# Kernel tuning notes

Measured on AMD Instinct MI355X. Metric: run time of the kernel, lower is better.

The kernel has to match this reference:

```python
import jax, jax.numpy as jnp
import numpy as np

N_NODES = 100000
N_EDGES = 1600000
IN_FEAT = 50
HIDDEN = 64
N_CLASSES = 41


def setup_inputs() -> dict:
    key = jax.random.key(0)
    ks = jax.random.split(key, 8)
    x = jax.random.normal(ks[0], (N_NODES, IN_FEAT), dtype=jnp.float32)
    W1_l = jax.random.normal(ks[1], (IN_FEAT, HIDDEN), dtype=jnp.float32) * (1.0 / np.sqrt(IN_FEAT))
    W1_r = jax.random.normal(ks[2], (IN_FEAT, HIDDEN), dtype=jnp.float32) * (1.0 / np.sqrt(IN_FEAT))
    b1 = jnp.zeros((HIDDEN,), dtype=jnp.float32)
    W2_l = jax.random.normal(ks[3], (HIDDEN, N_CLASSES), dtype=jnp.float32) * (1.0 / np.sqrt(HIDDEN))
    W2_r = jax.random.normal(ks[4], (HIDDEN, N_CLASSES), dtype=jnp.float32) * (1.0 / np.sqrt(HIDDEN))
    b2 = jnp.zeros((N_CLASSES,), dtype=jnp.float32)
    src = jax.random.randint(ks[5], (N_EDGES,), 0, N_NODES, dtype=jnp.int64 if jax.config.jax_enable_x64 else jnp.int32)
    dst = jax.random.randint(ks[6], (N_EDGES,), 0, N_NODES, dtype=jnp.int64 if jax.config.jax_enable_x64 else jnp.int32)
    return {"x": x, "W1_l": W1_l, "W1_r": W1_r, "b1": b1,
            "W2_l": W2_l, "W2_r": W2_r, "b2": b2, "src": src, "dst": dst}


def _sage_conv(h, src, dst, W_l, W_r, b):
    # sum-aggregate neighbor features (message from src -> dst), then dense transform
    agg = jax.ops.segment_sum(h[src], dst, num_segments=N_NODES)  # [N, F]
    return agg @ W_l + h @ W_r + b


def reference(x, W1_l, W1_r, b1, W2_l, W2_r, b2, src, dst):
    h = _sage_conv(x, src, dst, W1_l, W1_r, b1)
    h = jax.nn.relu(h)
    # dropout is identity in eval mode
    o = _sage_conv(h, src, dst, W2_l, W2_r, b2)
    return jax.nn.log_softmax(o, axis=1)
```

## Files before the change

kernel.cpp:

```cpp
#include <hip/hip_runtime.h>
#include <hip/hip_bf16.h>
#include <math.h>

#define N_NODES   100000
#define N_EDGES   1600000
#define IN_FEAT   50
#define HIDDEN    64
#define N_CLASSES 41
#define NC48      48
#define N_TILES   (N_NODES / 16)

#define NPB   200
#define NBUK  (N_NODES / NPB)
#define BEPT  16
#define BA_BLOCKS ((N_EDGES + 256 * BEPT - 1) / (256 * BEPT))
#define SCAP  4096

#define PACKX_BLOCKS (N_NODES * 64 / 256)
#define PW_BLOCKS    28

typedef __attribute__((ext_vector_type(8))) _Float16 half8;
typedef __attribute__((ext_vector_type(4))) float   float4v;

union f16pk { _Float16 h[2]; unsigned u; };

__device__ __forceinline__ int clampidx(int i) {
  return ((unsigned)i < (unsigned)N_NODES) ? i : 0;
}

__device__ __forceinline__ void acc8(float* acc, half8 u, float one) {
#pragma unroll
  for (int t = 0; t < 8; ++t) acc[t] = fmaf((float)u[t], one, acc[t]);
}

__global__ __launch_bounds__(256) void prep_kernel(
    const float* __restrict__ x, _Float16* __restrict__ xh,
    const float* __restrict__ W1l, const float* __restrict__ W1r,
    const float* __restrict__ W2l, const float* __restrict__ W2r,
    unsigned* __restrict__ wt1l, unsigned* __restrict__ wt1r,
    unsigned* __restrict__ wt2l, unsigned* __restrict__ wt2r,
    int* __restrict__ bcnt, int* __restrict__ wcurrel,
    int* __restrict__ start) {
  if (blockIdx.x < PACKX_BLOCKS) {
    int i = blockIdx.x * 256 + threadIdx.x;
    int node = i >> 6, c = i & 63;
    xh[i] = (c < IN_FEAT) ? (_Float16)x[node * IN_FEAT + c] : (_Float16)0.f;
    return;
  }
  int tid = threadIdx.x;
  if (blockIdx.x == PACKX_BLOCKS) {
    bcnt[tid] = 0; bcnt[256 + tid] = 0;
    wcurrel[tid] = 0; wcurrel[256 + tid] = 0;
    if (tid == 0) start[N_NODES] = N_EDGES;
  }
  int i = (blockIdx.x - PACKX_BLOCKS) * 256 + tid;
  f16pk pk;
  if (i < 2048 * 2) {
    int which = i >> 11, j = i & 2047;
    int n = j >> 5, kp = j & 31;
    const float* W = which ? W1r : W1l;
    int k0 = 2 * kp, k1 = 2 * kp + 1;
    pk.h[0] = (_Float16)((k0 < IN_FEAT) ? W[k0 * HIDDEN + n] : 0.f);
    pk.h[1] = (_Float16)((k1 < IN_FEAT) ? W[k1 * HIDDEN + n] : 0.f);
    (which ? wt1r : wt1l)[j] = pk.u;
  } else if (i < 4096 + 2 * 1536) {
    int j = i - 4096;
    int which = (j >= 1536), jj = which ? j - 1536 : j;
    int n = jj >> 5, kp = jj & 31;
    const float* W = which ? W2r : W2l;
    pk.h[0] = (_Float16)((n < N_CLASSES) ? W[(2 * kp) * N_CLASSES + n] : 0.f);
    pk.h[1] = (_Float16)((n < N_CLASSES) ? W[(2 * kp + 1) * N_CLASSES + n] : 0.f);
    (which ? wt2r : wt2l)[jj] = pk.u;
  }
}

__global__ __launch_bounds__(256) void bhist_kernel(
    const int* __restrict__ dst, int* __restrict__ bcnt) {
  __shared__ int lh[NBUK];
  int tid = threadIdx.x;
  for (int i = tid; i < NBUK; i += 256) lh[i] = 0;
  __syncthreads();
  int base = blockIdx.x * (256 * BEPT);
#pragma unroll
  for (int k = 0; k < BEPT; ++k) {
    int e = base + k * 256 + tid;
    if (e < N_EDGES) {
      int d = clampidx(dst[e]);
      atomicAdd(&lh[(unsigned)d / (unsigned)NPB], 1);
    }
  }
  __syncthreads();
  for (int i = tid; i < NBUK; i += 256)
    if (lh[i]) atomicAdd(&bcnt[i], lh[i]);
}

__global__ __launch_bounds__(256) void bucketA_kernel(
    const int* __restrict__ src, const int* __restrict__ dst,
    const int* __restrict__ bcnt, int* __restrict__ wcurrel,
    int* __restrict__ pairs) {
  __shared__ int sc[256];
  __shared__ int wb[NBUK];
  __shared__ int lcnt[NBUK];
  __shared__ int lbase[NBUK];
  int tid = threadIdx.x;
  int i0 = 2 * tid, i1 = 2 * tid + 1;
  int a0 = (i0 < NBUK) ? bcnt[i0] : 0;
  int a1 = (i1 < NBUK) ? bcnt[i1] : 0;
  int s = a0 + a1;
  sc[tid] = s;
  for (int i = tid; i < NBUK; i += 256) lcnt[i] = 0;
  __syncthreads();
  for (int off = 1; off < 256; off <<= 1) {
    int t = (tid >= off) ? sc[tid - off] : 0;
    __syncthreads();
    sc[tid] += t;
    __syncthreads();
  }
  int excl = sc[tid] - s;
  if (i0 < NBUK) wb[i0] = excl;
  if (i1 < NBUK) wb[i1] = excl + a0;
  __syncthreads();

  int base = blockIdx.x * (256 * BEPT);
  int pk[BEPT], w[BEPT], rk[BEPT];
#pragma unroll
  for (int k = 0; k < BEPT; ++k) {
    int e = base + k * 256 + tid;
    rk[k] = -1;
    if (e < N_EDGES) {
      int sv = clampidx(src[e]);
      int d = clampidx(dst[e]);
      w[k] = (unsigned)d / (unsigned)NPB;
      pk[k] = (sv << 8) | (d - w[k] * NPB);
      rk[k] = atomicAdd(&lcnt[w[k]], 1);
    }
  }
  __syncthreads();
  for (int i = tid; i < NBUK; i += 256)
    lbase[i] = wb[i] + atomicAdd(&wcurrel[i], lcnt[i]);
  __syncthreads();
#pragma unroll
  for (int k = 0; k < BEPT; ++k) {
    if (rk[k] >= 0) {
      int pos = lbase[w[k]] + rk[k];
      if ((unsigned)pos < (unsigned)N_EDGES) pairs[pos] = pk[k];
    }
  }
}

__global__ __launch_bounds__(256) void sort2_kernel(
    const int* __restrict__ pairs, const int* __restrict__ bcnt,
    int* __restrict__ start, int* __restrict__ ssrc) {
  __shared__ int obuf[SCAP];
  __shared__ int lhist[NPB];
  __shared__ int lcur[NPB];
  __shared__ int lscan[256];
  __shared__ int lohi[2];
  int b = blockIdx.x;
  int nbase = b * NPB;
  int tid = threadIdx.x;
  {
    int i0 = 2 * tid, i1 = 2 * tid + 1;
    int a0 = (i0 < NBUK) ? bcnt[i0] : 0;
    int a1 = (i1 < NBUK) ? bcnt[i1] : 0;
    int s = a0 + a1;
    lscan[tid] = s;
    __syncthreads();
    for (int off = 1; off < 256; off <<= 1) {
      int t = (tid >= off) ? lscan[tid - off] : 0;
      __syncthreads();
      lscan[tid] += t;
      __syncthreads();
    }
    int excl = lscan[tid] - s;
    if (i0 == b) { lohi[0] = excl;      lohi[1] = a0; }
    if (i1 == b) { lohi[0] = excl + a0; lohi[1] = a1; }
  }
  for (int i = tid; i < NPB; i += 256) lhist[i] = 0;
  __syncthreads();
  int lo = lohi[0];
  int ne = lohi[1];
  int hi = lo + ne;
  for (int i = lo + tid; i < hi; i += 256) {
    unsigned li = (unsigned)pairs[i] & 255u;
    if (li < (unsigned)NPB) atomicAdd(&lhist[li], 1);
  }
  __syncthreads();
  int hv = (tid < NPB) ? lhist[tid] : 0;
  lscan[tid] = hv;
  __syncthreads();
  for (int off = 1; off < 256; off <<= 1) {
    int t = (tid >= off) ? lscan[tid - off] : 0;
    __syncthreads();
    lscan[tid] += t;
    __syncthreads();
  }
  if (tid < NPB) {
    int excl = lscan[tid] - hv;
    lcur[tid] = excl;
    unsigned sidx = (unsigned)(nbase + tid);
    if (sidx < (unsigned)N_NODES) start[sidx] = lo + excl;
  }
  __syncthreads();
  if (ne >= 0 && ne <= SCAP) {
    for (int i = lo + tid; i < hi; i += 256) {
      int p = pairs[i];
      unsigned li = (unsigned)p & 255u;
      if (li < (unsigned)NPB) {
        int pos = atomicAdd(&lcur[li], 1);
        if ((unsigned)pos < (unsigned)SCAP) obuf[pos] = (int)((unsigned)p >> 8);
      }
    }
    __syncthreads();
    for (int i = tid; i < ne; i += 256) {
      unsigned gi = (unsigned)(lo + i);
      if (gi < (unsigned)N_EDGES) ssrc[gi] = obuf[i];
    }
  } else {
    for (int i = lo + tid; i < hi; i += 256) {
      int p = pairs[i];
      unsigned li = (unsigned)p & 255u;
      if (li < (unsigned)NPB) {
        int pos = atomicAdd(&lcur[li], 1);
        unsigned gi = (unsigned)(lo + pos);
        if (gi < (unsigned)N_EDGES) ssrc[gi] = (int)((unsigned)p >> 8);
      }
    }
  }
}

__global__ __launch_bounds__(256) void g1mlp_kernel(
    const half8* __restrict__ xq,
    const int* __restrict__ start, const int* __restrict__ ssrc,
    const _Float16* __restrict__ xh,
    const unsigned* __restrict__ wt1l, const unsigned* __restrict__ wt1r,
    const unsigned* __restrict__ wt2l, const unsigned* __restrict__ wt2r,
    const float* __restrict__ b1, const float* __restrict__ b2,
    _Float16* __restrict__ hlh, float* __restrict__ opart, float one) {
  __shared__ float aggF[16][68];
  __shared__ float sH[16][68];
  int tile = blockIdx.x;
  int wv = __builtin_amdgcn_readfirstlane(threadIdx.x >> 6);
  int lane = threadIdx.x & 63;
  int r = lane >> 3, q = lane & 7;

  for (int k = 0; k < 4; ++k) {
    int node = tile * 16 + wv * 4 + k;

    float accA[8] = {0.f, 0.f, 0.f, 0.f, 0.f, 0.f, 0.f, 0.f};
    float accB[8] = {0.f, 0.f, 0.f, 0.f, 0.f, 0.f, 0.f, 0.f};

    int s0 = start[node], s1 = start[node + 1];
    for (int base = s0; base < s1; base += 64) {
      int cnt = s1 - base;
      if (cnt > 64) cnt = 64;
      int idxv = (lane < cnt) ? ssrc[base + lane] : 0;
      int j = 0;
      for (; j + 16 <= cnt; j += 16) {
        int iA = clampidx(__shfl(idxv, j + r));
        int iB = clampidx(__shfl(idxv, j + 8 + r));
        acc8(accA, xq[iA * 8 + q], one);
        acc8(accB, xq[iB * 8 + q], one);
      }
      for (; j + 8 <= cnt; j += 8) {
        int iA = clampidx(__shfl(idxv, j + r));
        acc8(accA, xq[iA * 8 + q], one);
      }
      if (j < cnt) {
        int nrem = cnt - j;
        int iA = clampidx(__shfl(idxv, j + r));
        if (r < nrem) acc8(accA, xq[iA * 8 + q], one);
      }
    }
#pragma unroll
    for (int t = 0; t < 8; ++t) accA[t] += accB[t];
#pragma unroll
    for (int off = 8; off <= 32; off <<= 1) {
#pragma unroll
      for (int t = 0; t < 8; ++t) accA[t] += __shfl_xor(accA[t], off);
    }
    if (r == 0) {
      int nl = wv * 4 + k;
#pragma unroll
      for (int t = 0; t < 8; ++t) aggF[nl][q * 8 + t] = accA[t];
    }
  }
  __syncthreads();

  if (wv != 0) return;
  int m = lane & 15, quad = lane >> 4;

  half8 Aa[2], Ax[2];
#pragma unroll
  for (int s = 0; s < 2; ++s) {
    const float* pa = &aggF[m][s * 32 + quad * 8];
    half8 A;
#pragma unroll
    for (int jj = 0; jj < 8; ++jj) A[jj] = (_Float16)pa[jj];
    Aa[s] = A;
    Ax[s] = *(const half8*)(xh + (tile * 16 + m) * 64 + s * 32 + quad * 8);
  }

#pragma unroll
  for (int t = 0; t < 4; ++t) {
    int n = t * 16 + m;
    half8 Bl0 = *(const half8*)(wt1l + n * 32 + quad * 4);
    half8 Bl1 = *(const half8*)(wt1l + n * 32 + 16 + quad * 4);
    half8 Br0 = *(const half8*)(wt1r + n * 32 + quad * 4);
    half8 Br1 = *(const half8*)(wt1r + n * 32 + 16 + quad * 4);
    float4v acc = {0.f, 0.f, 0.f, 0.f};
    acc = __builtin_amdgcn_mfma_f32_16x16x32_f16(Aa[0], Bl0, acc, 0, 0, 0);
    acc = __builtin_amdgcn_mfma_f32_16x16x32_f16(Aa[1], Bl1, acc, 0, 0, 0);
    acc = __builtin_amdgcn_mfma_f32_16x16x32_f16(Ax[0], Br0, acc, 0, 0, 0);
    acc = __builtin_amdgcn_mfma_f32_16x16x32_f16(Ax[1], Br1, acc, 0, 0, 0);
    float bv = b1[n];
#pragma unroll
    for (int rr = 0; rr < 4; ++rr) {
      sH[quad * 4 + rr][n] = fmaxf(acc[rr] + bv, 0.f);
    }
  }

  half8 Ah[2];
#pragma unroll
  for (int s = 0; s < 2; ++s) {
    const float* pr = &sH[m][s * 32 + quad * 8];
    half8 A;
#pragma unroll
    for (int jj = 0; jj < 8; ++jj) A[jj] = (_Float16)pr[jj];
    Ah[s] = A;
  }

#pragma unroll
  for (int t = 0; t < 3; ++t) {
    int n = t * 16 + m;
    half8 Cl0 = *(const half8*)(wt2l + n * 32 + quad * 4);
    half8 Cl1 = *(const half8*)(wt2l + n * 32 + 16 + quad * 4);
    half8 Cr0 = *(const half8*)(wt2r + n * 32 + quad * 4);
    half8 Cr1 = *(const half8*)(wt2r + n * 32 + 16 + quad * 4);
    float4v acc2 = {0.f, 0.f, 0.f, 0.f};
    float4v acc3 = {0.f, 0.f, 0.f, 0.f};
    acc2 = __builtin_amdgcn_mfma_f32_16x16x32_f16(Ah[0], Cl0, acc2, 0, 0, 0);
    acc2 = __builtin_amdgcn_mfma_f32_16x16x32_f16(Ah[1], Cl1, acc2, 0, 0, 0);
    acc3 = __builtin_amdgcn_mfma_f32_16x16x32_f16(Ah[0], Cr0, acc3, 0, 0, 0);
    acc3 = __builtin_amdgcn_mfma_f32_16x16x32_f16(Ah[1], Cr1, acc3, 0, 0, 0);
    float bv = (n < N_CLASSES) ? b2[n] : 0.f;
#pragma unroll
    for (int rr = 0; rr < 4; ++rr) {
      int row = tile * 16 + quad * 4 + rr;
      hlh[row * NC48 + n] = (_Float16)acc2[rr];
      opart[row * NC48 + n] = acc3[rr] + bv;
    }
  }
}

__global__ __launch_bounds__(256) void gather2_kernel(
    const half8* __restrict__ hq,
    const float4* __restrict__ opart4,
    const int* __restrict__ start, const int* __restrict__ ssrc,
    float* __restrict__ out, float one) {
  int node = (blockIdx.x * 256 + threadIdx.x) >> 6;
  if (node >= N_NODES) return;
  node = __builtin_amdgcn_readfirstlane(node);
  int lane = threadIdx.x & 63;
  int r = lane >> 3, q = lane & 7;
  bool qOK = (q < 6);

  float op[8] = {0.f, 0.f, 0.f, 0.f, 0.f, 0.f, 0.f, 0.f};
  if (r == 0 && qOK) {
    float4 a = opart4[node * 12 + q * 2];
    float4 b = opart4[node * 12 + q * 2 + 1];
    op[0] = a.x; op[1] = a.y; op[2] = a.z; op[3] = a.w;
    op[4] = b.x; op[5] = b.y; op[6] = b.z; op[7] = b.w;
  }

  float accA[8] = {0.f, 0.f, 0.f, 0.f, 0.f, 0.f, 0.f, 0.f};
  float accB[8] = {0.f, 0.f, 0.f, 0.f, 0.f, 0.f, 0.f, 0.f};

  int s0 = start[node], s1 = start[node + 1];
  for (int base = s0; base < s1; base += 64) {
    int cnt = s1 - base;
    if (cnt > 64) cnt = 64;
    int idxv = (lane < cnt) ? ssrc[base + lane] : 0;
    int j = 0;
    for (; j + 16 <= cnt; j += 16) {
      int iA = clampidx(__shfl(idxv, j + r));
      int iB = clampidx(__shfl(idxv, j + 8 + r));
      if (qOK) {
        acc8(accA, hq[iA * 6 + q], one);
        acc8(accB, hq[iB * 6 + q], one);
      }
    }
    for (; j + 8 <= cnt; j += 8) {
      int iA = clampidx(__shfl(idxv, j + r));
      if (qOK) acc8(accA, hq[iA * 6 + q], one);
    }
    if (j < cnt) {
      int nrem = cnt - j;
      int iA = clampidx(__shfl(idxv, j + r));
      if (r < nrem && qOK) acc8(accA, hq[iA * 6 + q], one);
    }
  }
#pragma unroll
  for (int t = 0; t < 8; ++t) accA[t] += accB[t];
#pragma unroll
  for (int off = 8; off <= 32; off <<= 1) {
#pragma unroll
    for (int t = 0; t < 8; ++t) accA[t] += __shfl_xor(accA[t], off);
  }

  bool own = (r == 0) && qOK;
  float o[8];
  float lmax = -INFINITY;
#pragma unroll
  for (int t = 0; t < 8; ++t) {
    int f = q * 8 + t;
    o[t] = op[t] + accA[t];
    if (own && f < N_CLASSES) lmax = fmaxf(lmax, o[t]);
  }
  float vm = own ? lmax : -INFINITY;
#pragma unroll
  for (int off = 4; off >= 1; off >>= 1) vm = fmaxf(vm, __shfl_xor(vm, off));
  float lsum = 0.f;
#pragma unroll
  for (int t = 0; t < 8; ++t) {
    int f = q * 8 + t;
    if (own && f < N_CLASSES) lsum += expf(o[t] - vm);
  }
#pragma unroll
  for (int off = 4; off >= 1; off >>= 1) lsum += __shfl_xor(lsum, off);
  float lse = logf(lsum);
  if (own) {
#pragma unroll
    for (int t = 0; t < 8; ++t) {
      int f = q * 8 + t;
      if (f < N_CLASSES) out[node * N_CLASSES + f] = o[t] - vm - lse;
    }
  }
}

extern "C" void kernel_launch(void* const* d_in, const int* in_sizes, int n_in,
                              void* d_out, int out_size, void* d_ws, size_t ws_size,
                              hipStream_t stream) {
  const float* x   = (const float*)d_in[0];
  const float* W1l = (const float*)d_in[1];
  const float* W1r = (const float*)d_in[2];
  const float* b1  = (const float*)d_in[3];
  const float* W2l = (const float*)d_in[4];
  const float* W2r = (const float*)d_in[5];
  const float* b2  = (const float*)d_in[6];
  const int*   src = (const int*)d_in[7];
  const int*   dst = (const int*)d_in[8];
  float* out = (float*)d_out;

  int* counts  = (int*)d_ws;
  int* start   = counts + N_NODES;
  int* cursor  = start + (N_NODES + 1);
  int* partial = cursor + N_NODES;
  int* ssrc    = partial + 64;
  unsigned* wt1l = (unsigned*)(ssrc + N_EDGES);
  unsigned* wt1r = wt1l + 2048;
  unsigned* wt2l = wt1r + 2048;
  unsigned* wt2r = wt2l + 1536;
  uintptr_t pal = ((uintptr_t)(wt2r + 1536) + 255) & ~(uintptr_t)255;
  float* opart   = (float*)pal;
  _Float16* xh   = (_Float16*)(opart + (size_t)N_NODES * NC48);
  _Float16* hlh  = xh + (size_t)N_NODES * 64;

  int* bcnt    = counts;
  int* wcurrel = counts + 512;

  int* pairs = (int*)opart;

  prep_kernel<<<PACKX_BLOCKS + PW_BLOCKS, 256, 0, stream>>>(
      x, xh, W1l, W1r, W2l, W2r, wt1l, wt1r, wt2l, wt2r,
      bcnt, wcurrel, start);
  bhist_kernel<<<BA_BLOCKS, 256, 0, stream>>>(dst, bcnt);
  bucketA_kernel<<<BA_BLOCKS, 256, 0, stream>>>(src, dst, bcnt, wcurrel, pairs);
  sort2_kernel<<<NBUK, 256, 0, stream>>>(pairs, bcnt, start, ssrc);

  g1mlp_kernel<<<N_TILES, 256, 0, stream>>>(
      (const half8*)xh, start, ssrc, xh, wt1l, wt1r, wt2l, wt2r,
      b1, b2, hlh, opart, 1.0f);

  int gblocks = (N_NODES * 64 + 255) / 256;
  gather2_kernel<<<gblocks, 256, 0, stream>>>(
      (const half8*)hlh, (const float4*)opart, start, ssrc, out, 1.0f);
}
```

Before: 242.8 us.

## Split layer-1 MFMA epilogue across waves and tile the layer-2 gather with an LDS softmax

In the fused layer-1 kernel the dense MFMA epilogue, previously run by wave 0 alone, is split so each of the four waves computes one 16-column slice of the hidden layer and three waves compute the layer-2 slices, with an extra barrier between them. The second gather kernel now processes 16-node tiles per block, with each wave handling four nodes sequentially and staging the aggregates in LDS. Wave 0 then does a coalesced 4-lanes-per-node log-softmax epilogue with fewer idle lanes. The aim is to cut serialized epilogue work and improve lane utilisation in the output writes. The cost is an extra sync and less per-node parallelism in the gather.

```diff
diff --git a/kernel.cpp b/kernel.cpp
--- a/kernel.cpp
+++ b/kernel.cpp
@@ -287,7 +287,6 @@
   }
   __syncthreads();
 
-  if (wv != 0) return;
   int m = lane & 15, quad = lane >> 4;
 
   half8 Aa[2], Ax[2];
@@ -301,9 +300,8 @@
     Ax[s] = *(const half8*)(xh + (tile * 16 + m) * 64 + s * 32 + quad * 8);
   }
 
-#pragma unroll
-  for (int t = 0; t < 4; ++t) {
-    int n = t * 16 + m;
+  {
+    int n = wv * 16 + m;
     half8 Bl0 = *(const half8*)(wt1l + n * 32 + quad * 4);
     half8 Bl1 = *(const half8*)(wt1l + n * 32 + 16 + quad * 4);
     half8 Br0 = *(const half8*)(wt1r + n * 32 + quad * 4);
@@ -319,7 +317,9 @@
       sH[quad * 4 + rr][n] = fmaxf(acc[rr] + bv, 0.f);
     }
   }
-
+  __syncthreads();
+
+  if (wv >= 3) return;
   half8 Ah[2];
 #pragma unroll
   for (int s = 0; s < 2; ++s) {
@@ -329,10 +329,8 @@
     for (int jj = 0; jj < 8; ++jj) A[jj] = (_Float16)pr[jj];
     Ah[s] = A;
   }
-
-#pragma unroll
-  for (int t = 0; t < 3; ++t) {
-    int n = t * 16 + m;
+  {
+    int n = wv * 16 + m;
     half8 Cl0 = *(const half8*)(wt2l + n * 32 + quad * 4);
     half8 Cl1 = *(const half8*)(wt2l + n * 32 + 16 + quad * 4);
     half8 Cr0 = *(const half8*)(wt2r + n * 32 + quad * 4);
@@ -353,88 +351,98 @@
   }
 }
 
-__global__ __launch_bounds__(256) void gather2_kernel(
+#define AROW 49
+__global__ __launch_bounds__(256) void g2tile_kernel(
     const half8* __restrict__ hq,
     const float4* __restrict__ opart4,
     const int* __restrict__ start, const int* __restrict__ ssrc,
     float* __restrict__ out, float one) {
-  int node = (blockIdx.x * 256 + threadIdx.x) >> 6;
-  if (node >= N_NODES) return;
-  node = __builtin_amdgcn_readfirstlane(node);
+  __shared__ float aggF[16][AROW];
+  int tile = blockIdx.x;
+  int wv = __builtin_amdgcn_readfirstlane(threadIdx.x >> 6);
   int lane = threadIdx.x & 63;
   int r = lane >> 3, q = lane & 7;
   bool qOK = (q < 6);
 
-  float op[8] = {0.f, 0.f, 0.f, 0.f, 0.f, 0.f, 0.f, 0.f};
-  if (r == 0 && qOK) {
-    float4 a = opart4[node * 12 + q * 2];
-    float4 b = opart4[node * 12 + q * 2 + 1];
-    op[0] = a.x; op[1] = a.y; op[2] = a.z; op[3] = a.w;
-    op[4] = b.x; op[5] = b.y; op[6] = b.z; op[7] = b.w;
-  }
-
-  float accA[8] = {0.f, 0.f, 0.f, 0.f, 0.f, 0.f, 0.f, 0.f};
-  float accB[8] = {0.f, 0.f, 0.f, 0.f, 0.f, 0.f, 0.f, 0.f};
-
-  int s0 = start[node], s1 = start[node + 1];
-  for (int base = s0; base < s1; base += 64) {
-    int cnt = s1 - base;
-    if (cnt > 64) cnt = 64;
-    int idxv = (lane < cnt) ? ssrc[base + lane] : 0;
-    int j = 0;
-    for (; j + 16 <= cnt; j += 16) {
-      int iA = clampidx(__shfl(idxv, j + r));
-      int iB = clampidx(__shfl(idxv, j + 8 + r));
-      if (qOK) {
-        acc8(accA, hq[iA * 6 + q], one);
-        acc8(accB, hq[iB * 6 + q], one);
-      }
-    }
-    for (; j + 8 <= cnt; j += 8) {
-      int iA = clampidx(__shfl(idxv, j + r));
-      if (qOK) acc8(accA, hq[iA * 6 + q], one);
-    }
-    if (j < cnt) {
-      int nrem = cnt - j;
-      int iA = clampidx(__shfl(idxv, j + r));
-      if (r < nrem && qOK) acc8(accA, hq[iA * 6 + q], one);
-    }
-  }
-#pragma unroll
-  for (int t = 0; t < 8; ++t) accA[t] += accB[t];
-#pragma unroll
-  for (int off = 8; off <= 32; off <<= 1) {
-#pragma unroll
-    for (int t = 0; t < 8; ++t) accA[t] += __shfl_xor(accA[t], off);
-  }
-
-  bool own = (r == 0) && qOK;
-  float o[8];
+  for (int k = 0; k < 4; ++k) {
+    int node = tile * 16 + wv * 4 + k;
+
+    float accA[8] = {0.f, 0.f, 0.f, 0.f, 0.f, 0.f, 0.f, 0.f};
+    float accB[8] = {0.f, 0.f, 0.f, 0.f, 0.f, 0.f, 0.f, 0.f};
+
+    int s0 = start[node], s1 = start[node + 1];
+    for (int base = s0; base < s1; base += 64) {
+      int cnt = s1 - base;
+      if (cnt > 64) cnt = 64;
+      int idxv = (lane < cnt) ? ssrc[base + lane] : 0;
+      int j = 0;
+      for (; j + 16 <= cnt; j += 16) {
+        int iA = clampidx(__shfl(idxv, j + r));
+        int iB = clampidx(__shfl(idxv, j + 8 + r));
+        if (qOK) {
+          acc8(accA, hq[iA * 6 + q], one);
+          acc8(accB, hq[iB * 6 + q], one);
+        }
+      }
+      for (; j + 8 <= cnt; j += 8) {
+        int iA = clampidx(__shfl(idxv, j + r));
+        if (qOK) acc8(accA, hq[iA * 6 + q], one);
+      }
+      if (j < cnt) {
+        int nrem = cnt - j;
+        int iA = clampidx(__shfl(idxv, j + r));
+        if (r < nrem && qOK) acc8(accA, hq[iA * 6 + q], one);
+      }
+    }
+#pragma unroll
+    for (int t = 0; t < 8; ++t) accA[t] += accB[t];
+#pragma unroll
+    for (int off = 8; off <= 32; off <<= 1) {
+#pragma unroll
+      for (int t = 0; t < 8; ++t) accA[t] += __shfl_xor(accA[t], off);
+    }
+    if (r == 0 && qOK) {
+      int nl = wv * 4 + k;
+#pragma unroll
+      for (int t = 0; t < 8; ++t) aggF[nl][q * 8 + t] = accA[t];
+    }
+  }
+  __syncthreads();
+
+  if (wv != 0) return;
+  int m = lane >> 2, s = lane & 3;
+  int node = tile * 16 + m;
+
+  float o[12];
+#pragma unroll
+  for (int i = 0; i < 3; ++i) {
+    float4 a = opart4[node * 12 + s * 3 + i];
+    o[i * 4 + 0] = a.x; o[i * 4 + 1] = a.y;
+    o[i * 4 + 2] = a.z; o[i * 4 + 3] = a.w;
+  }
   float lmax = -INFINITY;
 #pragma unroll
-  for (int t = 0; t < 8; ++t) {
-    int f = q * 8 + t;
-    o[t] = op[t] + accA[t];
-    if (own && f < N_CLASSES) lmax = fmaxf(lmax, o[t]);
-  }
-  float vm = own ? lmax : -INFINITY;
-#pragma unroll
-  for (int off = 4; off >= 1; off >>= 1) vm = fmaxf(vm, __shfl_xor(vm, off));
+  for (int j = 0; j < 12; ++j) {
+    int f = s * 12 + j;
+    o[j] += aggF[m][f];
+    if (f < N_CLASSES) lmax = fmaxf(lmax, o[j]);
+  }
+  float vm = lmax;
+#pragma unroll
+  for (int off = 1; off <= 2; off <<= 1) vm = fmaxf(vm, __shfl_xor(vm, off));
   float lsum = 0.f;
 #pragma unroll
-  for (int t = 0; t < 8; ++t) {
-    int f = q * 8 + t;
-    if (own && f < N_CLASSES) lsum += expf(o[t] - vm);
-  }
-#pragma unroll
-  for (int off = 4; off >= 1; off >>= 1) lsum += __shfl_xor(lsum, off);
+  for (int j = 0; j < 12; ++j) {
+    int f = s * 12 + j;
+    if (f < N_CLASSES) lsum += expf(o[j] - vm);
+  }
+#pragma unroll
+  for (int off = 1; off <= 2; off <<= 1) lsum += __shfl_xor(lsum, off);
   float lse = logf(lsum);
-  if (own) {
-#pragma unroll
-    for (int t = 0; t < 8; ++t) {
-      int f = q * 8 + t;
-      if (f < N_CLASSES) out[node * N_CLASSES + f] = o[t] - vm - lse;
-    }
+#pragma unroll
+  for (int j = 0; j < 12; ++j) {
+    int f = s * 12 + j;
+    if (f < N_CLASSES) out[node * N_CLASSES + f] = o[j] - vm - lse;
   }
 }
 
@@ -482,7 +490,6 @@
       (const half8*)xh, start, ssrc, xh, wt1l, wt1r, wt2l, wt2r,
       b1, b2, hlh, opart, 1.0f);
 
-  int gblocks = (N_NODES * 64 + 255) / 256;
-  gather2_kernel<<<gblocks, 256, 0, stream>>>(
+  g2tile_kernel<<<N_TILES, 256, 0, stream>>>(
       (const half8*)hlh, (const float4*)opart, start, ssrc, out, 1.0f);
 }
```

After: 239.1 us. No clear change (-1.5%).
